# Performance work log

Measured on AMD Instinct MI355X. Metric: run time of the kernel, lower is better.

Reference implementation:

```python
import jax, jax.numpy as jnp
import numpy as np

CLARITY_K, CLARITY_SIGMA = 31, 8.0
TEXTURE_K, TEXTURE_SIGMA = 7, 1.5


def _gauss1d(size, sigma):
    grid = np.arange(size, dtype=np.float32) - size // 2
    g = np.exp(-grid ** 2 / (2.0 * sigma * sigma))
    return (g / g.sum()).astype(np.float32)


def _blur(img, g1d):
    # Separable Gaussian blur: the original 2D kernel is the outer product of
    # the normalized 1D gaussian with itself, so two 1D passes are exact.
    size = g1d.shape[0]
    pad = size // 2
    kh = jnp.asarray(g1d, img.dtype).reshape(1, 1, size, 1)  # OIHW, vertical
    kw = jnp.asarray(g1d, img.dtype).reshape(1, 1, 1, size)  # OIHW, horizontal
    dn = jax.lax.conv_dimension_numbers(img.shape, kh.shape, ('NCHW', 'OIHW', 'NCHW'))
    y = jax.lax.conv_general_dilated(img, kh, (1, 1), [(pad, pad), (0, 0)], dimension_numbers=dn)
    y = jax.lax.conv_general_dilated(y, kw, (1, 1), [(0, 0), (pad, pad)], dimension_numbers=dn)
    return y


def setup_inputs() -> dict:
    key = jax.random.key(0)
    kx, kc, kt = jax.random.split(key, 3)
    x = jax.random.uniform(kx, (8, 3, 1024, 1024), dtype=jnp.float32)
    clarity = jax.random.normal(kc, (), dtype=jnp.float32)
    texture = jax.random.normal(kt, (), dtype=jnp.float32)
    return {"x": x, "clarity": clarity, "texture": texture}


def reference(x, clarity, texture):
    g_clar = _gauss1d(CLARITY_K, CLARITY_SIGMA)
    g_tex = _gauss1d(TEXTURE_K, TEXTURE_SIGMA)

    # Rec.709 luma, shape [B,1,H,W]
    luma = 0.2126 * x[:, 0:1] + 0.7152 * x[:, 1:2] + 0.0722 * x[:, 2:3]

    mid_freq = luma - _blur(luma, g_clar)    # 31x31 gaussian
    high_freq = luma - _blur(luma, g_tex)    # 7x7 gaussian

    clarity_amount = jnp.tanh(clarity) * 0.5
    texture_amount = jnp.tanh(texture) * 0.3

    luma_enhanced = luma + clarity_amount * mid_freq + texture_amount * high_freq
    ratio = (luma_enhanced + 1e-6) / (luma + 1e-6)
    return jnp.clip(x * ratio, 0.0, 1.0)
```

## Files before the change

kernel.cpp:

```cpp
#include <hip/hip_runtime.h>
#include <hip/hip_fp16.h>
#include <cmath>

#define HH   1024
#define WW   1024
#define HW   (HH * WW)

#define SW    64
#define TH    128
#define T31R  158
#define T7R   134
#define SROWS 16
#define SPIT  96

constexpr double cexp(double v) {
    double term = 1.0, sum = 1.0;
    for (int i = 1; i < 64; ++i) { term *= v / (double)i; sum += term; }
    return sum;
}
struct GW { float g31[31]; float g7[7]; };
constexpr GW make_gw() {
    GW r{};
    double t31[31]; double s31 = 0.0;
    for (int i = 0; i < 31; ++i) { double d = (double)(i - 15); t31[i] = cexp(-d * d / 128.0); s31 += t31[i]; }
    for (int i = 0; i < 31; ++i) r.g31[i] = (float)(t31[i] / s31);
    double t7[7]; double s7 = 0.0;
    for (int i = 0; i < 7; ++i) { double d = (double)(i - 3); t7[i] = cexp(-d * d / 4.5); s7 += t7[i]; }
    for (int i = 0; i < 7; ++i) r.g7[i] = (float)(t7[i] / s7);
    return r;
}
__constant__ GW GWC = make_gw();

__global__ __launch_bounds__(256, 4)
void fused_tile(const float* __restrict__ x,
                const float* __restrict__ clar,
                const float* __restrict__ tex,
                float* __restrict__ out) {
    __shared__ __align__(16) __half t31s [T31R][SW];
    __shared__ __align__(16) __half t7s  [T7R][SW];
    __shared__ __align__(16) __half stage[SROWS][SPIT];

    const int id    = blockIdx.x;
    const int xcd   = id & 7;
    const int k     = id >> 3;
    const int combo = xcd * 16 + (k & 15);
    const int band  = k >> 4;
    const int img   = combo >> 4;
    const int strip = combo & 15;

    const int y0 = band * TH;
    const int x0 = strip * SW;
    const int t  = threadIdx.x;

    const float* xb = x   + (size_t)img * 3 * HW;
    float*       ob = out + (size_t)img * 3 * HW;

    for (int it = 0; it < 10; ++it) {
        const int gbase = it * SROWS;

        #pragma unroll
        for (int s = 0; s < 2; ++s) {
            const int u = t + 256 * s;
            if (u < 384) {
                const int r   = u / 24;
                const int c8  = u - 24 * r;
                const int tr  = gbase + r;
                const int y   = y0 - 15 + tr;
                const int col = x0 - 16 + 4 * c8;
                float4 L = make_float4(0.f, 0.f, 0.f, 0.f);
                if (tr < T31R && (unsigned)y < (unsigned)HH && (unsigned)col < (unsigned)WW) {
                    const float* xr = xb + (size_t)y * WW + col;
                    const float4 R  = *(const float4*)(xr);
                    const float4 G  = *(const float4*)(xr + HW);
                    const float4 Bc = *(const float4*)(xr + 2 * HW);
                    L.x = fmaf(0.2126f, R.x, fmaf(0.7152f, G.x, 0.0722f * Bc.x));
                    L.y = fmaf(0.2126f, R.y, fmaf(0.7152f, G.y, 0.0722f * Bc.y));
                    L.z = fmaf(0.2126f, R.z, fmaf(0.7152f, G.z, 0.0722f * Bc.z));
                    L.w = fmaf(0.2126f, R.w, fmaf(0.7152f, G.w, 0.0722f * Bc.w));
                }
                union { float2 f; __half2 h[2]; } W;
                W.h[0] = __floats2half2_rn(L.x, L.y);
                W.h[1] = __floats2half2_rn(L.z, L.w);
                *(float2*)&stage[r][4 * c8] = W.f;
            }
        }
        __syncthreads();

        {
            const int lr = t >> 4;
            const int c  = t & 15;
            const int tr = gbase + lr;
            if (tr < T31R) {
                float win[36];
                #pragma unroll
                for (int q = 0; q < 9; ++q) {
                    union { float2 f; __half2 h[2]; } U;
                    U.f = *(const float2*)&stage[lr][4 * c + 4 * q];
                    const float2 a = __half22float2(U.h[0]);
                    const float2 b = __half22float2(U.h[1]);
                    win[4 * q]     = a.x; win[4 * q + 1] = a.y;
                    win[4 * q + 2] = b.x; win[4 * q + 3] = b.y;
                }
                float o[4] = {0.f, 0.f, 0.f, 0.f};
                float p[4] = {0.f, 0.f, 0.f, 0.f};
                #pragma unroll
                for (int s = 0; s < 31; ++s) {
                    const float g = GWC.g31[s];
                    o[0] = fmaf(g, win[1 + s], o[0]);
                    o[1] = fmaf(g, win[2 + s], o[1]);
                    o[2] = fmaf(g, win[3 + s], o[2]);
                    o[3] = fmaf(g, win[4 + s], o[3]);
                }
                #pragma unroll
                for (int s = 0; s < 7; ++s) {
                    const float g = GWC.g7[s];
                    p[0] = fmaf(g, win[13 + s], p[0]);
                    p[1] = fmaf(g, win[14 + s], p[1]);
                    p[2] = fmaf(g, win[15 + s], p[2]);
                    p[3] = fmaf(g, win[16 + s], p[3]);
                }
                union { float2 f; __half2 h[2]; } W;
                W.h[0] = __floats2half2_rn(o[0], o[1]);
                W.h[1] = __floats2half2_rn(o[2], o[3]);
                *(float2*)&t31s[tr][4 * c] = W.f;
                if (tr >= 12 && tr < 12 + T7R) {
                    union { float2 f; __half2 h[2]; } V;
                    V.h[0] = __floats2half2_rn(p[0], p[1]);
                    V.h[1] = __floats2half2_rn(p[2], p[3]);
                    *(float2*)&t7s[tr - 12][4 * c] = V.f;
                }
            }
        }
        __syncthreads();
    }

    const float ca = tanhf(clar[0]) * 0.5f;
    const float ta = tanhf(tex[0]) * 0.3f;

    const int c = t & 63;
    #pragma unroll
    for (int s = 0; s < 2; ++s) {
        const int rg = (t >> 6) + 4 * s;
        const int r0 = rg * 16;

        float w31[31];
        #pragma unroll
        for (int q = 0; q < 30; ++q) w31[q] = __half2float(t31s[r0 + q][c]);
        float w7[7];
        #pragma unroll
        for (int q = 0; q < 6; ++q) w7[q] = __half2float(t7s[r0 + q][c]);

        #pragma unroll
        for (int j = 0; j < 16; ++j) {
            w31[(30 + j) % 31] = __half2float(t31s[r0 + 30 + j][c]);
            w7 [(6 + j) % 7]   = __half2float(t7s [r0 + 6 + j][c]);

            float a31 = 0.f;
            #pragma unroll
            for (int q = 0; q < 31; ++q)
                a31 = fmaf(GWC.g31[q], w31[(j + q) % 31], a31);
            float a7 = 0.f;
            #pragma unroll
            for (int q = 0; q < 7; ++q)
                a7 = fmaf(GWC.g7[q], w7[(j + q) % 7], a7);

            const int y = y0 + r0 + j;
            const float* px = xb + (size_t)y * WW + x0 + c;
            const float R  = px[0];
            const float G  = px[HW];
            const float Bc = px[2 * HW];

            const float L     = fmaf(0.2126f, R, fmaf(0.7152f, G, 0.0722f * Bc));
            const float le    = L + ca * (L - a31) + ta * (L - a7);
            const float ratio = (le + 1e-6f) / (L + 1e-6f);

            float* qo = ob + (size_t)y * WW + x0 + c;
            qo[0]      = fminf(fmaxf(R  * ratio, 0.f), 1.f);
            qo[HW]     = fminf(fmaxf(G  * ratio, 0.f), 1.f);
            qo[2 * HW] = fminf(fmaxf(Bc * ratio, 0.f), 1.f);
        }
    }
}

extern "C" void kernel_launch(void* const* d_in, const int* in_sizes, int n_in,
                              void* d_out, int out_size, void* d_ws, size_t ws_size,
                              hipStream_t stream) {
    const float* x    = (const float*)d_in[0];
    const float* clar = (const float*)d_in[1];
    const float* tex  = (const float*)d_in[2];
    float* out = (float*)d_out;

    dim3 grid(8 * 16 * 8);
    dim3 block(256);
    hipLaunchKernelGGL(fused_tile, grid, block, 0, stream, x, clar, tex, out);
}
```

Before: 200.1 us.

## Prefetch next input rows into registers and vectorize vertical pass to float2

```diff
diff --git a/kernel.cpp b/kernel.cpp
--- a/kernel.cpp
+++ b/kernel.cpp
@@ -55,38 +55,72 @@
     const float* xb = x   + (size_t)img * 3 * HW;
     float*       ob = out + (size_t)img * 3 * HW;
 
+    const int r0u = t / 24;
+    const int c80 = t - 24 * r0u;
+    const int u1  = t + 256;
+    const int r1u = u1 / 24;
+    const int c81 = u1 - 24 * r1u;
+    const bool has1 = (t < 128);
+    const int col0 = x0 - 16 + 4 * c80;
+    const int col1 = x0 - 16 + 4 * c81;
+    const bool c0ok = (unsigned)col0 < (unsigned)WW;
+    const bool c1ok = (unsigned)col1 < (unsigned)WW;
+
+    float4 R0, G0, B0, R1, G1, B1;
+
+    auto issue = [&](int it) {
+        const int gbase = it * SROWS;
+        {
+            const int tr = gbase + r0u;
+            const int y  = y0 - 15 + tr;
+            if (tr < T31R && (unsigned)y < (unsigned)HH && c0ok) {
+                const float* xr = xb + (size_t)y * WW + col0;
+                R0 = *(const float4*)(xr);
+                G0 = *(const float4*)(xr + HW);
+                B0 = *(const float4*)(xr + 2 * HW);
+            } else {
+                R0 = make_float4(0.f, 0.f, 0.f, 0.f); G0 = R0; B0 = R0;
+            }
+        }
+        if (has1) {
+            const int tr = gbase + r1u;
+            const int y  = y0 - 15 + tr;
+            if (tr < T31R && (unsigned)y < (unsigned)HH && c1ok) {
+                const float* xr = xb + (size_t)y * WW + col1;
+                R1 = *(const float4*)(xr);
+                G1 = *(const float4*)(xr + HW);
+                B1 = *(const float4*)(xr + 2 * HW);
+            } else {
+                R1 = make_float4(0.f, 0.f, 0.f, 0.f); G1 = R1; B1 = R1;
+            }
+        }
+    };
+
+    issue(0);
+
     for (int it = 0; it < 10; ++it) {
-        const int gbase = it * SROWS;
-
-        #pragma unroll
-        for (int s = 0; s < 2; ++s) {
-            const int u = t + 256 * s;
-            if (u < 384) {
-                const int r   = u / 24;
-                const int c8  = u - 24 * r;
-                const int tr  = gbase + r;
-                const int y   = y0 - 15 + tr;
-                const int col = x0 - 16 + 4 * c8;
-                float4 L = make_float4(0.f, 0.f, 0.f, 0.f);
-                if (tr < T31R && (unsigned)y < (unsigned)HH && (unsigned)col < (unsigned)WW) {
-                    const float* xr = xb + (size_t)y * WW + col;
-                    const float4 R  = *(const float4*)(xr);
-                    const float4 G  = *(const float4*)(xr + HW);
-                    const float4 Bc = *(const float4*)(xr + 2 * HW);
-                    L.x = fmaf(0.2126f, R.x, fmaf(0.7152f, G.x, 0.0722f * Bc.x));
-                    L.y = fmaf(0.2126f, R.y, fmaf(0.7152f, G.y, 0.0722f * Bc.y));
-                    L.z = fmaf(0.2126f, R.z, fmaf(0.7152f, G.z, 0.0722f * Bc.z));
-                    L.w = fmaf(0.2126f, R.w, fmaf(0.7152f, G.w, 0.0722f * Bc.w));
-                }
-                union { float2 f; __half2 h[2]; } W;
-                W.h[0] = __floats2half2_rn(L.x, L.y);
-                W.h[1] = __floats2half2_rn(L.z, L.w);
-                *(float2*)&stage[r][4 * c8] = W.f;
+        {
+            union { float2 f; __half2 h[2]; } W;
+            W.h[0] = __floats2half2_rn(fmaf(0.2126f, R0.x, fmaf(0.7152f, G0.x, 0.0722f * B0.x)),
+                                       fmaf(0.2126f, R0.y, fmaf(0.7152f, G0.y, 0.0722f * B0.y)));
+            W.h[1] = __floats2half2_rn(fmaf(0.2126f, R0.z, fmaf(0.7152f, G0.z, 0.0722f * B0.z)),
+                                       fmaf(0.2126f, R0.w, fmaf(0.7152f, G0.w, 0.0722f * B0.w)));
+            *(float2*)&stage[r0u][4 * c80] = W.f;
+            if (has1) {
+                union { float2 f; __half2 h[2]; } V;
+                V.h[0] = __floats2half2_rn(fmaf(0.2126f, R1.x, fmaf(0.7152f, G1.x, 0.0722f * B1.x)),
+                                           fmaf(0.2126f, R1.y, fmaf(0.7152f, G1.y, 0.0722f * B1.y)));
+                V.h[1] = __floats2half2_rn(fmaf(0.2126f, R1.z, fmaf(0.7152f, G1.z, 0.0722f * B1.z)),
+                                           fmaf(0.2126f, R1.w, fmaf(0.7152f, G1.w, 0.0722f * B1.w)));
+                *(float2*)&stage[r1u][4 * c81] = V.f;
             }
         }
         __syncthreads();
 
+        if (it + 1 < 10) issue(it + 1);
+
         {
+            const int gbase = it * SROWS;
             const int lr = t >> 4;
             const int c  = t & 15;
             const int tr = gbase + lr;
@@ -137,48 +171,75 @@
     const float ca = tanhf(clar[0]) * 0.5f;
     const float ta = tanhf(tex[0]) * 0.3f;
 
-    const int c = t & 63;
+    const int cc = (t & 31) * 2;
+    const int rg = t >> 5;
+    const int r0 = rg * 16;
+
+    float2 w31[31];
     #pragma unroll
-    for (int s = 0; s < 2; ++s) {
-        const int rg = (t >> 6) + 4 * s;
-        const int r0 = rg * 16;
-
-        float w31[31];
+    for (int q = 0; q < 30; ++q)
+        w31[q] = __half22float2(*(const __half2*)&t31s[r0 + q][cc]);
+    float2 w7[7];
+    #pragma unroll
+    for (int q = 0; q < 6; ++q)
+        w7[q] = __half22float2(*(const __half2*)&t7s[r0 + q][cc]);
+
+    {
+    const float* p0 = xb + (size_t)(y0 + r0) * WW + x0 + cc;
+    float2 R  = *(const float2*)(p0);
+    float2 G  = *(const float2*)(p0 + HW);
+    float2 Bc = *(const float2*)(p0 + 2 * HW);
+
+    #pragma unroll
+    for (int j = 0; j < 16; ++j) {
+        w31[(30 + j) % 31] = __half22float2(*(const __half2*)&t31s[r0 + 30 + j][cc]);
+        w7 [(6 + j) % 7]   = __half22float2(*(const __half2*)&t7s [r0 + 6 + j][cc]);
+
+        float2 Rn, Gn, Bn;
+        if (j < 15) {
+            const float* pn = xb + (size_t)(y0 + r0 + j + 1) * WW + x0 + cc;
+            Rn = *(const float2*)(pn);
+            Gn = *(const float2*)(pn + HW);
+            Bn = *(const float2*)(pn + 2 * HW);
+        }
+
+        float2 a31 = make_float2(0.f, 0.f);
         #pragma unroll
-        for (int q = 0; q < 30; ++q) w31[q] = __half2float(t31s[r0 + q][c]);
-        float w7[7];
+        for (int q = 0; q < 31; ++q) {
+            const float g = GWC.g31[q];
+            const float2 w = w31[(j + q) % 31];
+            a31.x = fmaf(g, w.x, a31.x);
+            a31.y = fmaf(g, w.y, a31.y);
+        }
+        float2 a7 = make_float2(0.f, 0.f);
         #pragma unroll
-        for (int q = 0; q < 6; ++q) w7[q] = __half2float(t7s[r0 + q][c]);
-
-        #pragma unroll
-        for (int j = 0; j < 16; ++j) {
-            w31[(30 + j) % 31] = __half2float(t31s[r0 + 30 + j][c]);
-            w7 [(6 + j) % 7]   = __half2float(t7s [r0 + 6 + j][c]);
-
-            float a31 = 0.f;
-            #pragma unroll
-            for (int q = 0; q < 31; ++q)
-                a31 = fmaf(GWC.g31[q], w31[(j + q) % 31], a31);
-            float a7 = 0.f;
-            #pragma unroll
-            for (int q = 0; q < 7; ++q)
-                a7 = fmaf(GWC.g7[q], w7[(j + q) % 7], a7);
-
-            const int y = y0 + r0 + j;
-            const float* px = xb + (size_t)y * WW + x0 + c;
-            const float R  = px[0];
-            const float G  = px[HW];
-            const float Bc = px[2 * HW];
-
-            const float L     = fmaf(0.2126f, R, fmaf(0.7152f, G, 0.0722f * Bc));
-            const float le    = L + ca * (L - a31) + ta * (L - a7);
-            const float ratio = (le + 1e-6f) / (L + 1e-6f);
-
-            float* qo = ob + (size_t)y * WW + x0 + c;
-            qo[0]      = fminf(fmaxf(R  * ratio, 0.f), 1.f);
-            qo[HW]     = fminf(fmaxf(G  * ratio, 0.f), 1.f);
-            qo[2 * HW] = fminf(fmaxf(Bc * ratio, 0.f), 1.f);
-        }
+        for (int q = 0; q < 7; ++q) {
+            const float g = GWC.g7[q];
+            const float2 w = w7[(j + q) % 7];
+            a7.x = fmaf(g, w.x, a7.x);
+            a7.y = fmaf(g, w.y, a7.y);
+        }
+
+        const int y = y0 + r0 + j;
+        float* qo = ob + (size_t)y * WW + x0 + cc;
+
+        const float Lx = fmaf(0.2126f, R.x, fmaf(0.7152f, G.x, 0.0722f * Bc.x));
+        const float Ly = fmaf(0.2126f, R.y, fmaf(0.7152f, G.y, 0.0722f * Bc.y));
+        const float lex = Lx + ca * (Lx - a31.x) + ta * (Lx - a7.x);
+        const float ley = Ly + ca * (Ly - a31.y) + ta * (Ly - a7.y);
+        const float rx = (lex + 1e-6f) / (Lx + 1e-6f);
+        const float ry = (ley + 1e-6f) / (Ly + 1e-6f);
+
+        float2 o0, o1, o2;
+        o0.x = fminf(fmaxf(R.x  * rx, 0.f), 1.f);  o0.y = fminf(fmaxf(R.y  * ry, 0.f), 1.f);
+        o1.x = fminf(fmaxf(G.x  * rx, 0.f), 1.f);  o1.y = fminf(fmaxf(G.y  * ry, 0.f), 1.f);
+        o2.x = fminf(fmaxf(Bc.x * rx, 0.f), 1.f);  o2.y = fminf(fmaxf(Bc.y * ry, 0.f), 1.f);
+        *(float2*)(qo)          = o0;
+        *(float2*)(qo + HW)     = o1;
+        *(float2*)(qo + 2 * HW) = o2;
+
+        if (j < 15) { R = Rn; G = Gn; Bc = Bn; }
+    }
     }
 }
 
```

Result: no change. 197.2 us (-1.4%).
